# Kernel optimization log

Hardware: AMD Instinct MI355X
Metric: run time of the kernel (lower is better)

The kernel has to match this reference:

```python
import jax, jax.numpy as jnp
import numpy as np

N_BUS = 4096
BATCH = 1024


def setup_inputs() -> dict:
    key = jax.random.key(0)
    ks = jax.random.split(key, 10)
    u = jax.random.normal(ks[0], (BATCH, N_BUS), dtype=jnp.float32)
    w = jax.random.normal(ks[1], (BATCH, N_BUS), dtype=jnp.float32)
    # parameters (torch.rand -> uniform[0,1); Linear init ~ U(-1/sqrt(n), 1/sqrt(n)))
    G = jax.random.uniform(ks[2], (N_BUS, N_BUS), dtype=jnp.float32)
    B = jax.random.uniform(ks[3], (N_BUS, N_BUS), dtype=jnp.float32)
    bias_p = jax.random.uniform(ks[4], (1, N_BUS), dtype=jnp.float32)
    bias_q = jax.random.uniform(ks[5], (1, N_BUS), dtype=jnp.float32)
    lim = 1.0 / np.sqrt(N_BUS)
    Wp = jax.random.uniform(ks[6], (N_BUS, N_BUS), dtype=jnp.float32, minval=-lim, maxval=lim)
    bp = jax.random.uniform(ks[7], (N_BUS,), dtype=jnp.float32, minval=-lim, maxval=lim)
    Wq = jax.random.uniform(ks[8], (N_BUS, N_BUS), dtype=jnp.float32, minval=-lim, maxval=lim)
    bq = jax.random.uniform(ks[9], (N_BUS,), dtype=jnp.float32, minval=-lim, maxval=lim)
    return {"u": u, "w": w, "G": G, "B": B, "bias_p": bias_p, "bias_q": bias_q,
            "Wp": Wp, "bp": bp, "Wq": Wq, "bq": bq}


def reference(u, w, G, B, bias_p, bias_q, Wp, bp, Wq, bq):
    # Algebraically identical to the original's outer-product form:
    # p_i = sum_k (u_i u_k + w_i w_k) G_ik + (w_i u_k - u_i w_k) B_ik
    #     = u_i (G u)_i + w_i (G w)_i + w_i (B u)_i - u_i (B w)_i
    # q_i = sum_k (w_i u_k - u_i w_k) G_ik - (u_i u_k + w_i w_k) B_ik
    #     = w_i (G u)_i - u_i (G w)_i - u_i (B u)_i - w_i (B w)_i
    Gu = u @ G.T  # (batch, n_bus): (G u)_i = sum_k G_ik u_k
    Gw = w @ G.T
    Bu = u @ B.T
    Bw = w @ B.T
    p = u * Gu + w * Gw + w * Bu - u * Bw + bias_p
    q = w * Gu - u * Gw - u * Bu - w * Bw + bias_q
    # nn.Linear: y = x @ W^T + b
    p = p @ Wp.T + bp
    q = q @ Wq.T + bq
    return (p, q)
```

## Files before the change

### kernel.cpp

```cpp
#include <hip/hip_runtime.h>
#include <hip/hip_bf16.h>

#define NB 4096
#define MB 1024
#define SZ ((size_t)MB * NB)
#define NN ((size_t)NB * NB)

typedef __bf16 bf16_t;
typedef __attribute__((ext_vector_type(8))) __bf16 bf16x8;
typedef __attribute__((ext_vector_type(4))) float f32x4;
typedef __attribute__((ext_vector_type(4))) unsigned int u32x4;

#define AS1 __attribute__((address_space(1)))
#define AS3 __attribute__((address_space(3)))
#define GLOAD16(gp, lp)                                                        \
  __builtin_amdgcn_global_load_lds((const AS1 unsigned int*)(gp),              \
                                   (AS3 unsigned int*)(lp), 16, 0, 0)
#define SBAR() __builtin_amdgcn_s_barrier()
#define SCHEDB() __builtin_amdgcn_sched_barrier(0)
#define MFMA16(a, b, c) __builtin_amdgcn_mfma_f32_16x16x32_bf16((a), (b), (c), 0, 0, 0)


__device__ __forceinline__ bf16x8 neg8(bf16x8 x) {
  u32x4 t;
  __builtin_memcpy(&t, &x, 16);
  t ^= 0x80008000u;
  bf16x8 y;
  __builtin_memcpy(&y, &t, 16);
  return y;
}

__device__ __forceinline__ bf16x8 cvt8(float4 a, float4 b) {
  bf16x8 v;
  v[0] = (bf16_t)a.x; v[1] = (bf16_t)a.y; v[2] = (bf16_t)a.z; v[3] = (bf16_t)a.w;
  v[4] = (bf16_t)b.x; v[5] = (bf16_t)b.y; v[6] = (bf16_t)b.z; v[7] = (bf16_t)b.w;
  return v;
}

#define ITEM_S (SZ / 8)
#define ITEM_N (NN / 8)

__global__ __launch_bounds__(256) void prep6_kernel(
    const float* __restrict__ u, const float* __restrict__ w,
    const float* __restrict__ G, const float* __restrict__ Bm,
    const float* __restrict__ Wp, const float* __restrict__ Wq,
    bf16_t* __restrict__ ws) {
  size_t stride = (size_t)gridDim.x * blockDim.x;
  const size_t tot = 2 * ITEM_S + 4 * ITEM_N;
  for (size_t i = (size_t)blockIdx.x * blockDim.x + threadIdx.x; i < tot;
       i += stride) {
    const float* src;
    bf16_t* dst;
    size_t off;
    if (i < ITEM_S) { src = u; dst = ws; off = i; }
    else if (i < 2 * ITEM_S) { src = w; dst = ws + SZ; off = i - ITEM_S; }
    else if (i < 2 * ITEM_S + ITEM_N) { src = G; dst = ws + 2 * SZ; off = i - 2 * ITEM_S; }
    else if (i < 2 * ITEM_S + 2 * ITEM_N) { src = Bm; dst = ws + 2 * SZ + NN; off = i - 2 * ITEM_S - ITEM_N; }
    else if (i < 2 * ITEM_S + 3 * ITEM_N) { src = Wp; dst = ws + 2 * SZ + 2 * NN; off = i - 2 * ITEM_S - 2 * ITEM_N; }
    else { src = Wq; dst = ws + 2 * SZ + 3 * NN; off = i - 2 * ITEM_S - 3 * ITEM_N; }
    const float4* s = reinterpret_cast<const float4*>(src) + off * 2;
    reinterpret_cast<bf16x8*>(dst)[off] = cvt8(s[0], s[1]);
  }
}

__global__ __launch_bounds__(256) void prep4_kernel(
    const float* __restrict__ u, const float* __restrict__ w,
    const float* __restrict__ G, const float* __restrict__ Bm,
    bf16_t* __restrict__ ws) {
  size_t stride = (size_t)gridDim.x * blockDim.x;
  const size_t tot = 2 * ITEM_S + 2 * ITEM_N;
  for (size_t i = (size_t)blockIdx.x * blockDim.x + threadIdx.x; i < tot;
       i += stride) {
    const float* src;
    bf16_t* dst;
    size_t off;
    if (i < ITEM_S) { src = u; dst = ws; off = i; }
    else if (i < 2 * ITEM_S) { src = w; dst = ws + SZ; off = i - ITEM_S; }
    else if (i < 2 * ITEM_S + ITEM_N) { src = G; dst = ws + 2 * SZ; off = i - 2 * ITEM_S; }
    else { src = Bm; dst = ws + 2 * SZ + NN; off = i - 2 * ITEM_S - ITEM_N; }
    const float4* s = reinterpret_cast<const float4*>(src) + off * 2;
    reinterpret_cast<bf16x8*>(dst)[off] = cvt8(s[0], s[1]);
  }
}

__global__ __launch_bounds__(512, 2) void fused1_v6(
    const float* __restrict__ u, const float* __restrict__ w,
    const bf16_t* __restrict__ ubf, const bf16_t* __restrict__ wbf,
    const bf16_t* __restrict__ Gbf, const bf16_t* __restrict__ Bbf,
    const float* __restrict__ bias_p, const float* __restrict__ bias_q,
    bf16_t* __restrict__ pq) {
  __shared__ bf16_t lds[4][4][128 * 32];
  const int tid = threadIdx.x, lane = tid & 63, wv = tid >> 6;
  const int bid = blockIdx.x;
  const int t = (bid & 7) * 32 + (bid >> 3);
  const int row0 = (t & 7) * 128, col0 = (t >> 3) * 128;
  const int wm = (wv >> 2) * 64, wn = (wv & 3) * 32;
  const int lr = lane & 15, kq = lane >> 4;
  const int kswz = (kq ^ ((lr >> 1) & 3)) << 3;

  const int srow = wv * 16 + (lane >> 2);
  const int sc = (lane & 3) ^ ((lane >> 3) & 3);
  const bf16_t* gsrc[4];
  gsrc[0] = ubf + (size_t)(row0 + srow) * NB + sc * 8;
  gsrc[1] = wbf + (size_t)(row0 + srow) * NB + sc * 8;
  gsrc[2] = Gbf + (size_t)(col0 + srow) * NB + sc * 8;
  gsrc[3] = Bbf + (size_t)(col0 + srow) * NB + sc * 8;

#define F1_ISS(op, sl, ko) GLOAD16(gsrc[op] + (ko), &lds[sl][op][wv * 512])

  int aoff[4], boff[2];
#pragma unroll
  for (int m = 0; m < 4; ++m) aoff[m] = (wm + m * 16 + lr) * 32 + kswz;
#pragma unroll
  for (int n = 0; n < 2; ++n) boff[n] = (wn + n * 16 + lr) * 32 + kswz;

  f32x4 aS[4][2] = {}, aT[4][2] = {};

#pragma unroll
  for (int hh = 0; hh < 3; ++hh) {
    F1_ISS(0, hh, hh * 32);
    F1_ISS(1, hh, hh * 32);
    F1_ISS(2, hh, hh * 32);
    F1_ISS(3, hh, hh * 32);
  }
  asm volatile("s_waitcnt vmcnt(8)" ::: "memory");
  SBAR();
  SCHEDB();

  const int HTOT = 2 * (NB / 64);
  for (int h = 0; h < HTOT; ++h) {
    const int slot = h & 3;
    const bool pf = (h + 3) < HTOT;
    const int pslot = (h + 3) & 3;
    const int pko = (h + 3) * 32;

    bf16x8 bG[2], bB[2], au[4], aw[4];
#pragma unroll
    for (int n = 0; n < 2; ++n) {
      bG[n] = *reinterpret_cast<const bf16x8*>(&lds[slot][2][boff[n]]);
      bB[n] = *reinterpret_cast<const bf16x8*>(&lds[slot][3][boff[n]]);
    }
#pragma unroll
    for (int m = 0; m < 4; ++m) {
      au[m] = *reinterpret_cast<const bf16x8*>(&lds[slot][0][aoff[m]]);
      aw[m] = *reinterpret_cast<const bf16x8*>(&lds[slot][1][aoff[m]]);
    }
    if (pf) {
      F1_ISS(0, pslot, pko);
      F1_ISS(1, pslot, pko);
      F1_ISS(2, pslot, pko);
      F1_ISS(3, pslot, pko);
    }
    bf16x8 bBn[2] = {neg8(bB[0]), neg8(bB[1])};
#pragma unroll
    for (int m = 0; m < 4; ++m)
#pragma unroll
      for (int n = 0; n < 2; ++n) {
        aS[m][n] = MFMA16(au[m], bG[n], aS[m][n]);
        aS[m][n] = MFMA16(aw[m], bBn[n], aS[m][n]);
        aT[m][n] = MFMA16(aw[m], bG[n], aT[m][n]);
        aT[m][n] = MFMA16(au[m], bB[n], aT[m][n]);
      }
    if (h < HTOT - 3)
      asm volatile("s_waitcnt vmcnt(8)" ::: "memory");
    else if (h == HTOT - 3)
      asm volatile("s_waitcnt vmcnt(4)" ::: "memory");
    else if (h == HTOT - 2)
      asm volatile("s_waitcnt vmcnt(0)" ::: "memory");
    SBAR();
    SCHEDB();
  }

  const int fr = lane & 15, fq = kq;
#pragma unroll
  for (int m = 0; m < 4; ++m)
#pragma unroll
    for (int n = 0; n < 2; ++n)
#pragma unroll
      for (int j = 0; j < 4; ++j) {
        int r = row0 + wm + m * 16 + fq * 4 + j;
        int c = col0 + wn + n * 16 + fr;
        size_t idx = (size_t)r * NB + c;
        float U = u[idx], W = w[idx];
        float S = aS[m][n][j], T = aT[m][n][j];
        pq[idx] = (bf16_t)(U * S + W * T + bias_p[c]);
        pq[SZ + idx] = (bf16_t)(W * S - U * T + bias_q[c]);
      }
}

__global__ __launch_bounds__(512, 2) void gemm2_v7(
    const bf16_t* __restrict__ pq, const bf16_t* __restrict__ Wpb,
    const bf16_t* __restrict__ Wqb, const float* __restrict__ bp,
    const float* __restrict__ bq, float* __restrict__ out) {
  __shared__ bf16_t lA[4][128 * 32];
  __shared__ bf16_t lW[4][256 * 32];
  const int tid = threadIdx.x, lane = tid & 63, wv = tid >> 6;
  const int bid = blockIdx.x;
  const int t = (bid & 7) * 32 + (bid >> 3);
  const int z = t >> 7;
  const int s = t & 127;
  const int row0 = (s & 7) * 128, col0 = (s >> 3) * 256;

  const bf16_t* A = pq + (size_t)z * SZ;
  const bf16_t* Wm = z ? Wqb : Wpb;
  const float* bias = z ? bq : bp;
  float* C = out + (size_t)z * SZ;

  const int wm = (wv >> 2) * 64, wn = (wv & 3) * 64;
  const int lr = lane & 15, kq = lane >> 4;
  const int kswz = (kq ^ ((lr >> 1) & 3)) << 3;

  const int srow = lane >> 2;
  const int sc = (lane & 3) ^ ((lane >> 3) & 3);
  const bf16_t* gA0 = A + (size_t)(row0 + wv * 16 + srow) * NB + sc * 8;
  const bf16_t* gW0 = Wm + (size_t)(col0 + wv * 32 + srow) * NB + sc * 8;
  const bf16_t* gW1 = gW0 + (size_t)16 * NB;

#define G2_ISS(sl, ko)                                                         \
  do {                                                                         \
    GLOAD16(gA0 + (ko), &lA[sl][wv * 512]);                                    \
    GLOAD16(gW0 + (ko), &lW[sl][wv * 1024]);                                   \
    GLOAD16(gW1 + (ko), &lW[sl][wv * 1024 + 512]);                             \
  } while (0)

  int aoff[4], woff[4];
#pragma unroll
  for (int m = 0; m < 4; ++m) aoff[m] = (wm + m * 16 + lr) * 32 + kswz;
#pragma unroll
  for (int n = 0; n < 4; ++n) woff[n] = (wn + n * 16 + lr) * 32 + kswz;

  f32x4 acc[4][4] = {};

#pragma unroll
  for (int hh = 0; hh < 3; ++hh) G2_ISS(hh, hh * 32);
  asm volatile("s_waitcnt vmcnt(6)" ::: "memory");
  SBAR();
  SCHEDB();

  const int HTOT = 2 * (NB / 64);
  for (int h = 0; h < HTOT; ++h) {
    const int slot = h & 3;
    const bool pf = (h + 3) < HTOT;
    const int pslot = (h + 3) & 3;
    const int pko = (h + 3) * 32;

    bf16x8 av[4], bw[4];
#pragma unroll
    for (int m = 0; m < 4; ++m)
      av[m] = *reinterpret_cast<const bf16x8*>(&lA[slot][aoff[m]]);
#pragma unroll
    for (int n = 0; n < 4; ++n)
      bw[n] = *reinterpret_cast<const bf16x8*>(&lW[slot][woff[n]]);
    if (pf) G2_ISS(pslot, pko);
#pragma unroll
    for (int m = 0; m < 4; ++m)
#pragma unroll
      for (int n = 0; n < 4; ++n)
        acc[m][n] = MFMA16(av[m], bw[n], acc[m][n]);
    if (h < HTOT - 3)
      asm volatile("s_waitcnt vmcnt(6)" ::: "memory");
    else if (h == HTOT - 3)
      asm volatile("s_waitcnt vmcnt(3)" ::: "memory");
    else if (h == HTOT - 2)
      asm volatile("s_waitcnt vmcnt(0)" ::: "memory");
    SBAR();
    SCHEDB();
  }

  const int fr = lane & 15, fq = kq;
#pragma unroll
  for (int m = 0; m < 4; ++m)
#pragma unroll
    for (int n = 0; n < 4; ++n)
#pragma unroll
      for (int j = 0; j < 4; ++j) {
        int r = row0 + wm + m * 16 + fq * 4 + j;
        int c = col0 + wn + n * 16 + fr;
        C[(size_t)r * NB + c] = acc[m][n][j] + bias[c];
      }
}

__device__ __forceinline__ int swz_off32(int r, int kk) {
  return r * 32 + ((kk ^ ((r >> 1) & 3)) << 3);
}

__device__ __forceinline__ void fb_stage_f32(const float* __restrict__ src,
                                             int row0, int k0, bf16_t* lds, int t) {
  int r = t >> 2, kk = t & 3;
  const float* p = src + (size_t)(row0 + r) * NB + k0 + (kk << 3);
  float4 v0 = *reinterpret_cast<const float4*>(p);
  float4 v1 = *reinterpret_cast<const float4*>(p + 4);
  *reinterpret_cast<bf16x8*>(lds + swz_off32(r, kk)) = cvt8(v0, v1);
}

__global__ __launch_bounds__(256, 2) void fb_gemm2(
    const bf16_t* __restrict__ pq, const float* __restrict__ Wp,
    const float* __restrict__ Wq, const float* __restrict__ bp,
    const float* __restrict__ bq, float* __restrict__ out) {
  __shared__ bf16_t lA[128 * 32], lW[128 * 32];
  const int z = blockIdx.z;
  const bf16_t* A = pq + (size_t)z * SZ;
  const float* Wm = z ? Wq : Wp;
  const float* bias = z ? bq : bp;
  float* C = out + (size_t)z * SZ;
  const int tid = threadIdx.x;
  const int lane = tid & 63, wv = tid >> 6;
  const int wm = (wv >> 1) * 64, wn = (wv & 1) * 64;
  const int row0 = blockIdx.y * 128, col0 = blockIdx.x * 128;
  const int lr = lane & 15, kq = lane >> 4;
  const int fslot = (kq ^ ((lr >> 1) & 3)) << 3;
  f32x4 acc[4][4] = {};
  for (int kt = 0; kt < NB; kt += 32) {
#pragma unroll
    for (int p = 0; p < 2; ++p) {
      int cb = p * 256 + wv * 64;
      int ci = cb + lane;
      int r = ci >> 2, kl = ci & 3;
      int ks = kl ^ ((r >> 1) & 3);
      const bf16_t* g = A + (size_t)(row0 + r) * NB + kt + (ks << 3);
      GLOAD16(g, lA + cb * 8);
    }
#pragma unroll
    for (int p = 0; p < 2; ++p)
      fb_stage_f32(Wm, col0, kt, lW, p * 256 + tid);
    __syncthreads();
    bf16x8 af[4], bg[4];
#pragma unroll
    for (int m = 0; m < 4; ++m)
      af[m] = *reinterpret_cast<const bf16x8*>(lA + (wm + m * 16 + lr) * 32 + fslot);
#pragma unroll
    for (int n = 0; n < 4; ++n)
      bg[n] = *reinterpret_cast<const bf16x8*>(lW + (wn + n * 16 + lr) * 32 + fslot);
#pragma unroll
    for (int m = 0; m < 4; ++m)
#pragma unroll
      for (int n = 0; n < 4; ++n)
        acc[m][n] = MFMA16(af[m], bg[n], acc[m][n]);
    __syncthreads();
  }
  const int fr = lane & 15, fq = lane >> 4;
#pragma unroll
  for (int m = 0; m < 4; ++m)
#pragma unroll
    for (int n = 0; n < 4; ++n)
#pragma unroll
      for (int j = 0; j < 4; ++j) {
        int r = row0 + wm + m * 16 + fq * 4 + j;
        int c = col0 + wn + n * 16 + fr;
        C[(size_t)r * NB + c] = acc[m][n][j] + bias[c];
      }
}

__global__ __launch_bounds__(512, 2) void fb_fused1(
    const float* __restrict__ u, const float* __restrict__ w,
    const float* __restrict__ G, const float* __restrict__ Bm,
    const float* __restrict__ bias_p, const float* __restrict__ bias_q,
    bf16_t* __restrict__ pq) {
  __shared__ bf16_t lU[128 * 32], lW[128 * 32], lG[128 * 32], lB[128 * 32];
  const int tid = threadIdx.x;
  const int lane = tid & 63, wv = tid >> 6;
  const int wm = (wv >> 2) * 64, wn = (wv & 3) * 32;
  const int row0 = blockIdx.y * 128, col0 = blockIdx.x * 128;
  const int lr = lane & 15, kq = lane >> 4;
  const int fslot = (kq ^ ((lr >> 1) & 3)) << 3;
  f32x4 aS[4][2] = {}, aT[4][2] = {};
  for (int kt = 0; kt < NB; kt += 32) {
    fb_stage_f32(u, row0, kt, lU, tid);
    fb_stage_f32(w, row0, kt, lW, tid);
    fb_stage_f32(G, col0, kt, lG, tid);
    fb_stage_f32(Bm, col0, kt, lB, tid);
    __syncthreads();
    bf16x8 au[4], aw[4], bG[2], bB[2], bBn[2];
#pragma unroll
    for (int m = 0; m < 4; ++m) {
      int off = (wm + m * 16 + lr) * 32 + fslot;
      au[m] = *reinterpret_cast<const bf16x8*>(lU + off);
      aw[m] = *reinterpret_cast<const bf16x8*>(lW + off);
    }
#pragma unroll
    for (int n = 0; n < 2; ++n) {
      int off = (wn + n * 16 + lr) * 32 + fslot;
      bG[n] = *reinterpret_cast<const bf16x8*>(lG + off);
      bB[n] = *reinterpret_cast<const bf16x8*>(lB + off);
      bBn[n] = neg8(bB[n]);
    }
#pragma unroll
    for (int m = 0; m < 4; ++m)
#pragma unroll
      for (int n = 0; n < 2; ++n) {
        aS[m][n] = MFMA16(au[m], bG[n], aS[m][n]);
        aS[m][n] = MFMA16(aw[m], bBn[n], aS[m][n]);
        aT[m][n] = MFMA16(aw[m], bG[n], aT[m][n]);
        aT[m][n] = MFMA16(au[m], bB[n], aT[m][n]);
      }
    __syncthreads();
  }
  const int fr = lane & 15, fq = lane >> 4;
#pragma unroll
  for (int m = 0; m < 4; ++m)
#pragma unroll
    for (int n = 0; n < 2; ++n)
#pragma unroll
      for (int j = 0; j < 4; ++j) {
        int r = row0 + wm + m * 16 + fq * 4 + j;
        int c = col0 + wn + n * 16 + fr;
        size_t idx = (size_t)r * NB + c;
        float U = u[idx], W = w[idx];
        float S = aS[m][n][j], T = aT[m][n][j];
        pq[idx] = (bf16_t)(U * S + W * T + bias_p[c]);
        pq[SZ + idx] = (bf16_t)(W * S - U * T + bias_q[c]);
      }
}

extern "C" void kernel_launch(void* const* d_in, const int* in_sizes, int n_in,
                              void* d_out, int out_size, void* d_ws, size_t ws_size,
                              hipStream_t stream) {
  const float* u = (const float*)d_in[0];
  const float* w = (const float*)d_in[1];
  const float* G = (const float*)d_in[2];
  const float* Bm = (const float*)d_in[3];
  const float* bias_p = (const float*)d_in[4];
  const float* bias_q = (const float*)d_in[5];
  const float* Wp = (const float*)d_in[6];
  const float* bp = (const float*)d_in[7];
  const float* Wq = (const float*)d_in[8];
  const float* bq = (const float*)d_in[9];
  (void)in_sizes; (void)n_in; (void)out_size;

  const size_t need_full = (6 * SZ + 4 * NN) * sizeof(bf16_t);
  const size_t need_mid = (6 * SZ + 2 * NN) * sizeof(bf16_t);

  if (ws_size >= need_full) {
    bf16_t* ws = (bf16_t*)d_ws;
    bf16_t* ubf = ws;
    bf16_t* wbf = ws + SZ;
    bf16_t* Gbf = ws + 2 * SZ;
    bf16_t* Bbf = Gbf + NN;
    bf16_t* Wpb = Bbf + NN;
    bf16_t* Wqb = Wpb + NN;
    bf16_t* pqw = Wqb + NN;
    prep6_kernel<<<2048, 256, 0, stream>>>(u, w, G, Bm, Wp, Wq, ws);
    fused1_v6<<<256, 512, 0, stream>>>(u, w, ubf, wbf, Gbf, Bbf,
                                       bias_p, bias_q, pqw);
    gemm2_v7<<<256, 512, 0, stream>>>(pqw, Wpb, Wqb, bp, bq, (float*)d_out);
  } else if (ws_size >= need_mid) {
    bf16_t* ws = (bf16_t*)d_ws;
    bf16_t* ubf = ws;
    bf16_t* wbf = ws + SZ;
    bf16_t* Gbf = ws + 2 * SZ;
    bf16_t* Bbf = Gbf + NN;
    bf16_t* pqw = Bbf + NN;
    prep4_kernel<<<2048, 256, 0, stream>>>(u, w, G, Bm, ws);
    fused1_v6<<<256, 512, 0, stream>>>(u, w, ubf, wbf, Gbf, Bbf,
                                       bias_p, bias_q, pqw);
    fb_gemm2<<<dim3(NB / 128, MB / 128, 2), 256, 0, stream>>>(
        pqw, Wp, Wq, bp, bq, (float*)d_out);
  } else {
    bf16_t* pqw = (bf16_t*)d_ws;
    fb_fused1<<<dim3(NB / 128, MB / 128), 512, 0, stream>>>(
        u, w, G, Bm, bias_p, bias_q, pqw);
    fb_gemm2<<<dim3(NB / 128, MB / 128, 2), 256, 0, stream>>>(
        pqw, Wp, Wq, bp, bq, (float*)d_out);
  }
}
```

Baseline: 306.3 us.

## Double-buffer LDS fragment reads and retile second GEMM to 128x128 blocks

Both GEMM kernels now read the next k-slice's LDS fragments into a second register set before issuing the MFMAs on the current one. A manual 2x unrolled loop uses ping-pong fragment structs and a tighter vmcnt wait. The second GEMM moves from 512-thread blocks with 128x256 tiles to 256-thread blocks with 128x128 tiles, doubling the grid to 512 blocks. This is meant to hide LDS read latency behind MFMA work and improve occupancy and load balance, at the cost of more registers and more global re-reads of the A and W operands.

```diff
diff --git a/kernel.cpp b/kernel.cpp
--- a/kernel.cpp
+++ b/kernel.cpp
@@ -19,6 +19,8 @@
 #define SBAR() __builtin_amdgcn_s_barrier()
 #define SCHEDB() __builtin_amdgcn_sched_barrier(0)
 #define MFMA16(a, b, c) __builtin_amdgcn_mfma_f32_16x16x32_bf16((a), (b), (c), 0, 0, 0)
+#define VMCNT4() asm volatile("s_waitcnt vmcnt(4)" ::: "memory")
+#define VMCNT0() asm volatile("s_waitcnt vmcnt(0)" ::: "memory")
 
 
 __device__ __forceinline__ bf16x8 neg8(bf16x8 x) {
@@ -83,7 +85,10 @@
   }
 }
 
-__global__ __launch_bounds__(512, 2) void fused1_v6(
+struct F1Frag { bf16x8 au[4], aw[4], bG[2], bB[2]; };
+struct G2Frag { bf16x8 av[4], bw[4]; };
+
+__global__ __launch_bounds__(512, 2) void fused1_v7(
     const float* __restrict__ u, const float* __restrict__ w,
     const bf16_t* __restrict__ ubf, const bf16_t* __restrict__ wbf,
     const bf16_t* __restrict__ Gbf, const bf16_t* __restrict__ Bbf,
@@ -106,7 +111,15 @@
   gsrc[2] = Gbf + (size_t)(col0 + srow) * NB + sc * 8;
   gsrc[3] = Bbf + (size_t)(col0 + srow) * NB + sc * 8;
 
-#define F1_ISS(op, sl, ko) GLOAD16(gsrc[op] + (ko), &lds[sl][op][wv * 512])
+#define F1_ISSUE(hh)                                                           \
+  do {                                                                         \
+    const int _sl = (hh) & 3;                                                  \
+    const int _ko = (hh) * 32;                                                 \
+    GLOAD16(gsrc[0] + _ko, &lds[_sl][0][wv * 512]);                            \
+    GLOAD16(gsrc[1] + _ko, &lds[_sl][1][wv * 512]);                            \
+    GLOAD16(gsrc[2] + _ko, &lds[_sl][2][wv * 512]);                            \
+    GLOAD16(gsrc[3] + _ko, &lds[_sl][3][wv * 512]);                            \
+  } while (0)
 
   int aoff[4], boff[2];
 #pragma unroll
@@ -114,62 +127,65 @@
 #pragma unroll
   for (int n = 0; n < 2; ++n) boff[n] = (wn + n * 16 + lr) * 32 + kswz;
 
+#define F1_READ(F, sl)                                                         \
+  do {                                                                         \
+    const bf16_t* _b = &lds[sl][0][0];                                         \
+    _Pragma("unroll") for (int _n = 0; _n < 2; ++_n) {                         \
+      (F).bG[_n] = *reinterpret_cast<const bf16x8*>(_b + 2 * 4096 + boff[_n]); \
+      (F).bB[_n] = *reinterpret_cast<const bf16x8*>(_b + 3 * 4096 + boff[_n]); \
+    }                                                                          \
+    _Pragma("unroll") for (int _m = 0; _m < 4; ++_m) {                         \
+      (F).au[_m] = *reinterpret_cast<const bf16x8*>(_b + aoff[_m]);            \
+      (F).aw[_m] = *reinterpret_cast<const bf16x8*>(_b + 4096 + aoff[_m]);     \
+    }                                                                          \
+  } while (0)
+
+#define F1_MFMA(F)                                                             \
+  do {                                                                         \
+    bf16x8 _nB0 = neg8((F).bB[0]), _nB1 = neg8((F).bB[1]);                     \
+    _Pragma("unroll") for (int _m = 0; _m < 4; ++_m) {                         \
+      aS[_m][0] = MFMA16((F).au[_m], (F).bG[0], aS[_m][0]);                    \
+      aS[_m][0] = MFMA16((F).aw[_m], _nB0, aS[_m][0]);                         \
+      aT[_m][0] = MFMA16((F).aw[_m], (F).bG[0], aT[_m][0]);                    \
+      aT[_m][0] = MFMA16((F).au[_m], (F).bB[0], aT[_m][0]);                    \
+      aS[_m][1] = MFMA16((F).au[_m], (F).bG[1], aS[_m][1]);                    \
+      aS[_m][1] = MFMA16((F).aw[_m], _nB1, aS[_m][1]);                         \
+      aT[_m][1] = MFMA16((F).aw[_m], (F).bG[1], aT[_m][1]);                    \
+      aT[_m][1] = MFMA16((F).au[_m], (F).bB[1], aT[_m][1]);                    \
+    }                                                                          \
+  } while (0)
+
+#define F1_SYNC(hh)                                                            \
+  do {                                                                         \
+    if ((hh) <= 124) VMCNT4();                                                 \
+    else if ((hh) == 125) VMCNT0();                                            \
+    if ((hh) <= 125) SBAR();                                                   \
+    SCHEDB();                                                                  \
+  } while (0)
+
   f32x4 aS[4][2] = {}, aT[4][2] = {};
-
-#pragma unroll
-  for (int hh = 0; hh < 3; ++hh) {
-    F1_ISS(0, hh, hh * 32);
-    F1_ISS(1, hh, hh * 32);
-    F1_ISS(2, hh, hh * 32);
-    F1_ISS(3, hh, hh * 32);
-  }
-  asm volatile("s_waitcnt vmcnt(8)" ::: "memory");
+  F1Frag fA, fB;
+
+  F1_ISSUE(0); F1_ISSUE(1); F1_ISSUE(2);
+  VMCNT4();
   SBAR();
   SCHEDB();
-
-  const int HTOT = 2 * (NB / 64);
-  for (int h = 0; h < HTOT; ++h) {
-    const int slot = h & 3;
-    const bool pf = (h + 3) < HTOT;
-    const int pslot = (h + 3) & 3;
-    const int pko = (h + 3) * 32;
-
-    bf16x8 bG[2], bB[2], au[4], aw[4];
-#pragma unroll
-    for (int n = 0; n < 2; ++n) {
-      bG[n] = *reinterpret_cast<const bf16x8*>(&lds[slot][2][boff[n]]);
-      bB[n] = *reinterpret_cast<const bf16x8*>(&lds[slot][3][boff[n]]);
+  F1_READ(fA, 0);
+
+  for (int h = 0; h < 127; h += 2) {
+    F1_READ(fB, (h + 1) & 3);
+    if (h + 3 < 128) F1_ISSUE(h + 3);
+    F1_MFMA(fA);
+    F1_SYNC(h);
+    const int h1 = h + 1;
+    if (h1 < 127) {
+      F1_READ(fA, (h1 + 1) & 3);
+      if (h1 + 3 < 128) F1_ISSUE(h1 + 3);
+      F1_MFMA(fB);
+      F1_SYNC(h1);
     }
-#pragma unroll
-    for (int m = 0; m < 4; ++m) {
-      au[m] = *reinterpret_cast<const bf16x8*>(&lds[slot][0][aoff[m]]);
-      aw[m] = *reinterpret_cast<const bf16x8*>(&lds[slot][1][aoff[m]]);
-    }
-    if (pf) {
-      F1_ISS(0, pslot, pko);
-      F1_ISS(1, pslot, pko);
-      F1_ISS(2, pslot, pko);
-      F1_ISS(3, pslot, pko);
-    }
-    bf16x8 bBn[2] = {neg8(bB[0]), neg8(bB[1])};
-#pragma unroll
-    for (int m = 0; m < 4; ++m)
-#pragma unroll
-      for (int n = 0; n < 2; ++n) {
-        aS[m][n] = MFMA16(au[m], bG[n], aS[m][n]);
-        aS[m][n] = MFMA16(aw[m], bBn[n], aS[m][n]);
-        aT[m][n] = MFMA16(aw[m], bG[n], aT[m][n]);
-        aT[m][n] = MFMA16(au[m], bB[n], aT[m][n]);
-      }
-    if (h < HTOT - 3)
-      asm volatile("s_waitcnt vmcnt(8)" ::: "memory");
-    else if (h == HTOT - 3)
-      asm volatile("s_waitcnt vmcnt(4)" ::: "memory");
-    else if (h == HTOT - 2)
-      asm volatile("s_waitcnt vmcnt(0)" ::: "memory");
-    SBAR();
-    SCHEDB();
-  }
+  }
+  F1_MFMA(fB);
 
   const int fr = lane & 15, fq = kq;
 #pragma unroll
@@ -188,39 +204,42 @@
       }
 }
 
-__global__ __launch_bounds__(512, 2) void gemm2_v7(
+__global__ __launch_bounds__(256, 2) void gemm2_v8(
     const bf16_t* __restrict__ pq, const bf16_t* __restrict__ Wpb,
     const bf16_t* __restrict__ Wqb, const float* __restrict__ bp,
     const float* __restrict__ bq, float* __restrict__ out) {
-  __shared__ bf16_t lA[4][128 * 32];
-  __shared__ bf16_t lW[4][256 * 32];
+  __shared__ bf16_t lds[4][2][128 * 32];
   const int tid = threadIdx.x, lane = tid & 63, wv = tid >> 6;
   const int bid = blockIdx.x;
-  const int t = (bid & 7) * 32 + (bid >> 3);
-  const int z = t >> 7;
-  const int s = t & 127;
-  const int row0 = (s & 7) * 128, col0 = (s >> 3) * 256;
+  const int t = (bid & 7) * 64 + (bid >> 3);
+  const int z = t >> 8;
+  const int s = t & 255;
+  const int row0 = (s & 7) * 128, col0 = (s >> 3) * 128;
 
   const bf16_t* A = pq + (size_t)z * SZ;
   const bf16_t* Wm = z ? Wqb : Wpb;
   const float* bias = z ? bq : bp;
   float* C = out + (size_t)z * SZ;
 
-  const int wm = (wv >> 2) * 64, wn = (wv & 3) * 64;
+  const int wm = (wv >> 1) * 64, wn = (wv & 1) * 64;
   const int lr = lane & 15, kq = lane >> 4;
   const int kswz = (kq ^ ((lr >> 1) & 3)) << 3;
 
-  const int srow = lane >> 2;
-  const int sc = (lane & 3) ^ ((lane >> 3) & 3);
-  const bf16_t* gA0 = A + (size_t)(row0 + wv * 16 + srow) * NB + sc * 8;
-  const bf16_t* gW0 = Wm + (size_t)(col0 + wv * 32 + srow) * NB + sc * 8;
-  const bf16_t* gW1 = gW0 + (size_t)16 * NB;
-
-#define G2_ISS(sl, ko)                                                         \
-  do {                                                                         \
-    GLOAD16(gA0 + (ko), &lA[sl][wv * 512]);                                    \
-    GLOAD16(gW0 + (ko), &lW[sl][wv * 1024]);                                   \
-    GLOAD16(gW1 + (ko), &lW[sl][wv * 1024 + 512]);                             \
+  const int srow = tid >> 2;
+  const int sc = (tid & 3) ^ ((tid >> 3) & 3);
+  const bf16_t* gA0 = A + (size_t)(row0 + srow) * NB + sc * 8;
+  const bf16_t* gA1 = gA0 + (size_t)64 * NB;
+  const bf16_t* gW0 = Wm + (size_t)(col0 + srow) * NB + sc * 8;
+  const bf16_t* gW1 = gW0 + (size_t)64 * NB;
+
+#define G2_ISSUE(hh)                                                           \
+  do {                                                                         \
+    const int _sl = (hh) & 3;                                                  \
+    const int _ko = (hh) * 32;                                                 \
+    GLOAD16(gA0 + _ko, &lds[_sl][0][wv * 512]);                                \
+    GLOAD16(gA1 + _ko, &lds[_sl][0][2048 + wv * 512]);                         \
+    GLOAD16(gW0 + _ko, &lds[_sl][1][wv * 512]);                                \
+    GLOAD16(gW1 + _ko, &lds[_sl][1][2048 + wv * 512]);                         \
   } while (0)
 
   int aoff[4], woff[4];
@@ -229,43 +248,45 @@
 #pragma unroll
   for (int n = 0; n < 4; ++n) woff[n] = (wn + n * 16 + lr) * 32 + kswz;
 
+#define G2_READ(F, sl)                                                         \
+  do {                                                                         \
+    const bf16_t* _b = &lds[sl][0][0];                                         \
+    _Pragma("unroll") for (int _m = 0; _m < 4; ++_m)                           \
+        (F).av[_m] = *reinterpret_cast<const bf16x8*>(_b + aoff[_m]);          \
+    _Pragma("unroll") for (int _n = 0; _n < 4; ++_n)                           \
+        (F).bw[_n] = *reinterpret_cast<const bf16x8*>(_b + 4096 + woff[_n]);   \
+  } while (0)
+
+#define G2_MFMA(F)                                                             \
+  do {                                                                         \
+    _Pragma("unroll") for (int _m = 0; _m < 4; ++_m)                           \
+        _Pragma("unroll") for (int _n = 0; _n < 4; ++_n)                       \
+            acc[_m][_n] = MFMA16((F).av[_m], (F).bw[_n], acc[_m][_n]);         \
+  } while (0)
+
   f32x4 acc[4][4] = {};
-
-#pragma unroll
-  for (int hh = 0; hh < 3; ++hh) G2_ISS(hh, hh * 32);
-  asm volatile("s_waitcnt vmcnt(6)" ::: "memory");
+  G2Frag fA, fB;
+
+  G2_ISSUE(0); G2_ISSUE(1); G2_ISSUE(2);
+  VMCNT4();
   SBAR();
   SCHEDB();
-
-  const int HTOT = 2 * (NB / 64);
-  for (int h = 0; h < HTOT; ++h) {
-    const int slot = h & 3;
-    const bool pf = (h + 3) < HTOT;
-    const int pslot = (h + 3) & 3;
-    const int pko = (h + 3) * 32;
-
-    bf16x8 av[4], bw[4];
-#pragma unroll
-    for (int m = 0; m < 4; ++m)
-      av[m] = *reinterpret_cast<const bf16x8*>(&lA[slot][aoff[m]]);
-#pragma unroll
-    for (int n = 0; n < 4; ++n)
-      bw[n] = *reinterpret_cast<const bf16x8*>(&lW[slot][woff[n]]);
-    if (pf) G2_ISS(pslot, pko);
-#pragma unroll
-    for (int m = 0; m < 4; ++m)
-#pragma unroll
-      for (int n = 0; n < 4; ++n)
-        acc[m][n] = MFMA16(av[m], bw[n], acc[m][n]);
-    if (h < HTOT - 3)
-      asm volatile("s_waitcnt vmcnt(6)" ::: "memory");
-    else if (h == HTOT - 3)
-      asm volatile("s_waitcnt vmcnt(3)" ::: "memory");
-    else if (h == HTOT - 2)
-      asm volatile("s_waitcnt vmcnt(0)" ::: "memory");
-    SBAR();
-    SCHEDB();
-  }
+  G2_READ(fA, 0);
+
+  for (int h = 0; h < 127; h += 2) {
+    G2_READ(fB, (h + 1) & 3);
+    if (h + 3 < 128) G2_ISSUE(h + 3);
+    G2_MFMA(fA);
+    F1_SYNC(h);
+    const int h1 = h + 1;
+    if (h1 < 127) {
+      G2_READ(fA, (h1 + 1) & 3);
+      if (h1 + 3 < 128) G2_ISSUE(h1 + 3);
+      G2_MFMA(fB);
+      F1_SYNC(h1);
+    }
+  }
+  G2_MFMA(fB);
 
   const int fr = lane & 15, fq = kq;
 #pragma unroll
@@ -440,9 +461,9 @@
     bf16_t* Wqb = Wpb + NN;
     bf16_t* pqw = Wqb + NN;
     prep6_kernel<<<2048, 256, 0, stream>>>(u, w, G, Bm, Wp, Wq, ws);
-    fused1_v6<<<256, 512, 0, stream>>>(u, w, ubf, wbf, Gbf, Bbf,
+    fused1_v7<<<256, 512, 0, stream>>>(u, w, ubf, wbf, Gbf, Bbf,
                                        bias_p, bias_q, pqw);
-    gemm2_v7<<<256, 512, 0, stream>>>(pqw, Wpb, Wqb, bp, bq, (float*)d_out);
+    gemm2_v8<<<512, 256, 0, stream>>>(pqw, Wpb, Wqb, bp, bq, (float*)d_out);
   } else if (ws_size >= need_mid) {
     bf16_t* ws = (bf16_t*)d_ws;
     bf16_t* ubf = ws;
@@ -451,7 +472,7 @@
     bf16_t* Bbf = Gbf + NN;
     bf16_t* pqw = Bbf + NN;
     prep4_kernel<<<2048, 256, 0, stream>>>(u, w, G, Bm, ws);
-    fused1_v6<<<256, 512, 0, stream>>>(u, w, ubf, wbf, Gbf, Bbf,
+    fused1_v7<<<256, 512, 0, stream>>>(u, w, ubf, wbf, Gbf, Bbf,
                                        bias_p, bias_q, pqw);
     fb_gemm2<<<dim3(NB / 128, MB / 128, 2), 256, 0, stream>>>(
         pqw, Wp, Wq, bp, bq, (float*)d_out);
```

Measured after the change: 300.5 us. No clear change (-1.9%).

## Shrink second GEMM tile to 128x128 with 4 waves and staggered K start

Applied to the files above, without the earlier changes.

The second GEMM kernel changes from 256 blocks of 512 threads with 128x256 tiles to 512 blocks of 256 threads with 128x128 tiles. The LDS buffers are merged into one array, and the load-issue pattern and vmcnt waits are adjusted to four loads per stage. Odd blocks begin their K loop at a rotated offset so concurrent blocks read different K slices of the shared operands. This aims to improve CU occupancy and load balance across the 256 CUs and to reduce cache and channel contention, but each tile reuses its data less, so more global traffic is needed per FLOP.

```diff
diff --git a/kernel.cpp b/kernel.cpp
--- a/kernel.cpp
+++ b/kernel.cpp
@@ -19,6 +19,7 @@
 #define SBAR() __builtin_amdgcn_s_barrier()
 #define SCHEDB() __builtin_amdgcn_sched_barrier(0)
 #define MFMA16(a, b, c) __builtin_amdgcn_mfma_f32_16x16x32_bf16((a), (b), (c), 0, 0, 0)
+#define VMCNT(n) asm volatile("s_waitcnt vmcnt(" #n ")" ::: "memory")
 
 
 __device__ __forceinline__ bf16x8 neg8(bf16x8 x) {
@@ -123,7 +124,7 @@
     F1_ISS(2, hh, hh * 32);
     F1_ISS(3, hh, hh * 32);
   }
-  asm volatile("s_waitcnt vmcnt(8)" ::: "memory");
+  VMCNT(8);
   SBAR();
   SCHEDB();
 
@@ -162,11 +163,11 @@
         aT[m][n] = MFMA16(au[m], bB[n], aT[m][n]);
       }
     if (h < HTOT - 3)
-      asm volatile("s_waitcnt vmcnt(8)" ::: "memory");
+      VMCNT(8);
     else if (h == HTOT - 3)
-      asm volatile("s_waitcnt vmcnt(4)" ::: "memory");
+      VMCNT(4);
     else if (h == HTOT - 2)
-      asm volatile("s_waitcnt vmcnt(0)" ::: "memory");
+      VMCNT(0);
     SBAR();
     SCHEDB();
   }
@@ -188,39 +189,43 @@
       }
 }
 
-__global__ __launch_bounds__(512, 2) void gemm2_v7(
+__global__ __launch_bounds__(256, 2) void gemm2_v9(
     const bf16_t* __restrict__ pq, const bf16_t* __restrict__ Wpb,
     const bf16_t* __restrict__ Wqb, const float* __restrict__ bp,
     const float* __restrict__ bq, float* __restrict__ out) {
-  __shared__ bf16_t lA[4][128 * 32];
-  __shared__ bf16_t lW[4][256 * 32];
+  __shared__ bf16_t lds[4][2][128 * 32];
   const int tid = threadIdx.x, lane = tid & 63, wv = tid >> 6;
   const int bid = blockIdx.x;
-  const int t = (bid & 7) * 32 + (bid >> 3);
-  const int z = t >> 7;
-  const int s = t & 127;
-  const int row0 = (s & 7) * 128, col0 = (s >> 3) * 256;
+  const int t = (bid & 7) * 64 + (bid >> 3);
+  const int z = t >> 8;
+  const int s = t & 255;
+  const int row0 = (s & 7) * 128, col0 = (s >> 3) * 128;
+  const int koff = (bid & 1) << 6;
 
   const bf16_t* A = pq + (size_t)z * SZ;
   const bf16_t* Wm = z ? Wqb : Wpb;
   const float* bias = z ? bq : bp;
   float* C = out + (size_t)z * SZ;
 
-  const int wm = (wv >> 2) * 64, wn = (wv & 3) * 64;
+  const int wm = (wv >> 1) * 64, wn = (wv & 1) * 64;
   const int lr = lane & 15, kq = lane >> 4;
   const int kswz = (kq ^ ((lr >> 1) & 3)) << 3;
 
-  const int srow = lane >> 2;
-  const int sc = (lane & 3) ^ ((lane >> 3) & 3);
-  const bf16_t* gA0 = A + (size_t)(row0 + wv * 16 + srow) * NB + sc * 8;
-  const bf16_t* gW0 = Wm + (size_t)(col0 + wv * 32 + srow) * NB + sc * 8;
-  const bf16_t* gW1 = gW0 + (size_t)16 * NB;
-
-#define G2_ISS(sl, ko)                                                         \
+  const int srow = tid >> 2;
+  const int sc = (tid & 3) ^ ((tid >> 3) & 3);
+  const bf16_t* gA0 = A + (size_t)(row0 + srow) * NB + sc * 8;
+  const bf16_t* gA1 = gA0 + (size_t)64 * NB;
+  const bf16_t* gW0 = Wm + (size_t)(col0 + srow) * NB + sc * 8;
+  const bf16_t* gW1 = gW0 + (size_t)64 * NB;
+
+#define G2_ISSUE(hh)                                                           \
   do {                                                                         \
-    GLOAD16(gA0 + (ko), &lA[sl][wv * 512]);                                    \
-    GLOAD16(gW0 + (ko), &lW[sl][wv * 1024]);                                   \
-    GLOAD16(gW1 + (ko), &lW[sl][wv * 1024 + 512]);                             \
+    const int _sl = (hh) & 3;                                                  \
+    const int _ko = (((hh) + koff) & 127) * 32;                                \
+    GLOAD16(gA0 + _ko, &lds[_sl][0][wv * 512]);                                \
+    GLOAD16(gA1 + _ko, &lds[_sl][0][2048 + wv * 512]);                         \
+    GLOAD16(gW0 + _ko, &lds[_sl][1][wv * 512]);                                \
+    GLOAD16(gW1 + _ko, &lds[_sl][1][2048 + wv * 512]);                         \
   } while (0)
 
   int aoff[4], woff[4];
@@ -231,9 +236,8 @@
 
   f32x4 acc[4][4] = {};
 
-#pragma unroll
-  for (int hh = 0; hh < 3; ++hh) G2_ISS(hh, hh * 32);
-  asm volatile("s_waitcnt vmcnt(6)" ::: "memory");
+  G2_ISSUE(0); G2_ISSUE(1); G2_ISSUE(2);
+  VMCNT(4);
   SBAR();
   SCHEDB();
 
@@ -241,28 +245,26 @@
   for (int h = 0; h < HTOT; ++h) {
     const int slot = h & 3;
     const bool pf = (h + 3) < HTOT;
-    const int pslot = (h + 3) & 3;
-    const int pko = (h + 3) * 32;
 
     bf16x8 av[4], bw[4];
 #pragma unroll
     for (int m = 0; m < 4; ++m)
-      av[m] = *reinterpret_cast<const bf16x8*>(&lA[slot][aoff[m]]);
+      av[m] = *reinterpret_cast<const bf16x8*>(&lds[slot][0][aoff[m]]);
 #pragma unroll
     for (int n = 0; n < 4; ++n)
-      bw[n] = *reinterpret_cast<const bf16x8*>(&lW[slot][woff[n]]);
-    if (pf) G2_ISS(pslot, pko);
+      bw[n] = *reinterpret_cast<const bf16x8*>(&lds[slot][1][woff[n]]);
+    if (pf) G2_ISSUE(h + 3);
 #pragma unroll
     for (int m = 0; m < 4; ++m)
 #pragma unroll
       for (int n = 0; n < 4; ++n)
         acc[m][n] = MFMA16(av[m], bw[n], acc[m][n]);
     if (h < HTOT - 3)
-      asm volatile("s_waitcnt vmcnt(6)" ::: "memory");
+      VMCNT(4);
     else if (h == HTOT - 3)
-      asm volatile("s_waitcnt vmcnt(3)" ::: "memory");
+      VMCNT(2);
     else if (h == HTOT - 2)
-      asm volatile("s_waitcnt vmcnt(0)" ::: "memory");
+      VMCNT(0);
     SBAR();
     SCHEDB();
   }
@@ -442,7 +444,7 @@
     prep6_kernel<<<2048, 256, 0, stream>>>(u, w, G, Bm, Wp, Wq, ws);
     fused1_v6<<<256, 512, 0, stream>>>(u, w, ubf, wbf, Gbf, Bbf,
                                        bias_p, bias_q, pqw);
-    gemm2_v7<<<256, 512, 0, stream>>>(pqw, Wpb, Wqb, bp, bq, (float*)d_out);
+    gemm2_v9<<<512, 256, 0, stream>>>(pqw, Wpb, Wqb, bp, bq, (float*)d_out);
   } else if (ws_size >= need_mid) {
     bf16_t* ws = (bf16_t*)d_ws;
     bf16_t* ubf = ws;
```

Result: no change. 302.2 us (median of 2 runs) (-1.3%).
